# Performance work log

Measured on AMD Instinct MI355X. Metric: run time of the kernel, lower is better.

The kernel has to match this reference:

```python
import jax, jax.numpy as jnp
import numpy as np

NUM_EMB = 8192
DIM = 64
DECAY = 0.99
EPS = 1e-05
COMMIT = 0.25


def setup_inputs() -> dict:
    key = jax.random.key(0)
    k1, k2, k3 = jax.random.split(key, 3)
    inputs = jax.random.normal(k1, (8, 4096, DIM), jnp.float32)
    weight = jax.random.normal(k2, (NUM_EMB, DIM), jnp.float32)
    ema_cluster_count = jnp.ones((NUM_EMB,), jnp.float32)
    ema_weight_sum = jax.random.normal(k3, (NUM_EMB, DIM), jnp.float32)
    return {
        'inputs': inputs,
        'weight': weight,
        'ema_cluster_count': ema_cluster_count,
        'ema_weight_sum': ema_weight_sum,
    }


def reference(inputs, weight, ema_cluster_count, ema_weight_sum):
    flat = inputs.reshape(-1, DIM)  # [N, D]
    distances = (
        jnp.sum(flat ** 2, axis=1, keepdims=True)
        + jnp.sum(weight ** 2, axis=1)
        - 2.0 * flat @ weight.T
    )
    idx = jnp.argmin(distances, axis=1)  # [N] int

    # EMA stats (training branch): one-hot column sums == segment counts,
    # encodings.T @ flat == segment sums of inputs by code index.
    counts = jax.ops.segment_sum(
        jnp.ones(flat.shape[0], jnp.float32), idx, num_segments=NUM_EMB)
    new_cc = ema_cluster_count * DECAY + (1.0 - DECAY) * counts
    emb_sum = jax.ops.segment_sum(flat, idx, num_segments=NUM_EMB)
    new_ws = ema_weight_sum * DECAY + (1.0 - DECAY) * emb_sum

    n = jnp.sum(new_cc)
    smoothed = (new_cc + EPS) / (n + NUM_EMB * EPS) * n
    new_weight = new_ws / smoothed[:, None]  # updated codebook [K, D]

    quantized_raw = new_weight[idx].reshape(inputs.shape)
    e_latent_loss = jnp.mean((jax.lax.stop_gradient(quantized_raw) - inputs) ** 2)
    vq_loss = COMMIT * e_latent_loss

    avg_probs = counts / flat.shape[0]
    perplexity = jnp.exp(-jnp.sum(avg_probs * jnp.log(avg_probs + 1e-10)))

    # straight-through estimator
    quantized = inputs + jax.lax.stop_gradient(quantized_raw - inputs)
    return quantized, vq_loss, idx, perplexity, new_weight, new_cc, new_ws
```

## Files before the change

kernel.cpp:

```cpp
#include <hip/hip_runtime.h>
#include <math.h>

typedef _Float16 f16x8 __attribute__((ext_vector_type(8)));
typedef float f32x4 __attribute__((ext_vector_type(4)));

#define NROWS 32768
#define KEMB  8192

#define DECAYF 0.99f
#define OMDF   0.01f

#define OUT_Q    0
#define OUT_LOSS 2097152
#define OUT_IDX  2097153
#define OUT_PERP 2129921
#define OUT_NW   2129922
#define OUT_NCC  2654210
#define OUT_NWS  2662402

#define WS_N      0
#define WS_ENT    1
#define WS_COUNTS 4
#define WS_EMB    8196
#define WS_IDX    532484
#define WS_W2H    565252
#define WS_WFRAG  573444
#define WS_ZERO_UNITS 532484

__device__ __forceinline__ float sq_rn(float v) { return __fmul_rn(v, v); }

__device__ __forceinline__ float npsumsq64(const float* vbuf) {
  float a[8];
#pragma unroll
  for (int j = 0; j < 8; ++j) a[j] = sq_rn(vbuf[j]);
#pragma unroll
  for (int m = 1; m < 8; ++m)
#pragma unroll
    for (int j = 0; j < 8; ++j) a[j] = __fadd_rn(a[j], sq_rn(vbuf[m*8 + j]));
  return __fadd_rn(__fadd_rn(__fadd_rn(a[0],a[1]), __fadd_rn(a[2],a[3])),
                   __fadd_rn(__fadd_rn(a[4],a[5]), __fadd_rn(a[6],a[7])));
}

__device__ __forceinline__ void split_f16(float x, _Float16& hi, _Float16& lo) {
  hi = (_Float16)x;
  float r = __fsub_rn(x, (float)hi);
  lo = (_Float16)r;
}

__global__ __launch_bounds__(256) void prep_kernel(const float* __restrict__ wg,
                                                   float* __restrict__ ws) {
  const int tid = blockIdx.x * 256 + threadIdx.x;
  if (tid < KEMB) {
    const float* src = wg + (size_t)tid * 64;
    float vbuf[64];
#pragma unroll
    for (int f = 0; f < 16; ++f) {
      float4 v = *(const float4*)(src + f*4);
      vbuf[f*4+0]=v.x; vbuf[f*4+1]=v.y; vbuf[f*4+2]=v.z; vbuf[f*4+3]=v.w;
    }
    ws[WS_W2H + tid] = __fmul_rn(0.5f, npsumsq64(vbuf));
  } else if (tid < KEMB + 65536) {
    const int u = tid - KEMB;
    const int K = u >> 3, g = u & 7;
    const int n = K & 15, P = K >> 4;
    const int slot = (g&3)*16 + n, shi = g >> 2;
    const float* src = wg + (size_t)K*64 + g*8;
    float4 v0 = *(const float4*)src, v1 = *(const float4*)(src + 4);
    float vv[8] = {v0.x,v0.y,v0.z,v0.w,v1.x,v1.y,v1.z,v1.w};
    f16x8 hi, lo;
#pragma unroll
    for (int j = 0; j < 8; ++j) { _Float16 h, l; split_f16(vv[j], h, l); hi[j]=h; lo[j]=l; }
    _Float16* wf = (_Float16*)(ws + WS_WFRAG);
    *(f16x8*)&wf[((size_t)(P*4 + shi)*64 + slot)*8]     = hi;
    *(f16x8*)&wf[((size_t)(P*4 + 2 + shi)*64 + slot)*8] = lo;
  }
}

__global__ __launch_bounds__(1024, 4) void argmin_kernel(const float* __restrict__ xg,
                                                         float* __restrict__ out,
                                                         float* __restrict__ ws) {
  __shared__ __align__(16) _Float16 xp[8*4*64*8];
  __shared__ float md[128*8];
  __shared__ int   mk[128*8];
  __shared__ int   bkL[128];

  const int t    = threadIdx.x;
  const int lane = t & 63, wv = t >> 6;
  const int quad = lane >> 4, n16 = lane & 15;
  const int rg = wv >> 3, cg = wv & 7;
  const int row0 = blockIdx.x * 128;
  const _Float16* __restrict__ wfrag = (const _Float16*)(ws + WS_WFRAG);
  const float* __restrict__ w2hg = ws + WS_W2H;

  {
    const int u  = t;
    const int rp = u >> 7, n = (u >> 3) & 15, g = u & 7;
    const float* src = xg + (size_t)(row0 + rp*16 + n)*64 + g*8;
    float4 v0 = *(const float4*)src, v1 = *(const float4*)(src + 4);
    float vv[8] = {v0.x,v0.y,v0.z,v0.w,v1.x,v1.y,v1.z,v1.w};
    f16x8 hi, lo;
#pragma unroll
    for (int j = 0; j < 8; ++j) { _Float16 h, l; split_f16(-vv[j], h, l); hi[j]=h; lo[j]=l; }
    const int slot = (g&3)*16 + n, shi = g >> 2;
    *(f16x8*)&xp[(((rp*4) + shi)*64 + slot)*8]     = hi;
    *(f16x8*)&xp[(((rp*4) + 2 + shi)*64 + slot)*8] = lo;
  }
  __syncthreads();

  f16x8 b[4][4];
#pragma unroll
  for (int bt = 0; bt < 4; ++bt)
#pragma unroll
    for (int s = 0; s < 4; ++s)
      b[bt][s] = *(const f16x8*)&xp[(((rg*4+bt)*4 + s)*64 + lane)*8];

  float bestd[4]; int bestk[4];
#pragma unroll
  for (int i = 0; i < 4; ++i) { bestd[i] = INFINITY; bestk[i] = 0; }

  const size_t lane8 = (size_t)lane * 8;
  const int q4 = quad * 4;

  f16x8 wh0, wh1, wl0, wl1;
  int kb = cg;
  {
    const size_t base = (size_t)kb * 2048 + lane8;
    wh0 = *(const f16x8*)&wfrag[base];
    wh1 = *(const f16x8*)&wfrag[base + 512];
    wl0 = *(const f16x8*)&wfrag[base + 1024];
    wl1 = *(const f16x8*)&wfrag[base + 1536];
  }
  float4 cw = *(const float4*)&w2hg[kb*16 + q4];

#pragma unroll 1
  for (int it = 0; it < 64; ++it) {
    const f32x4 cin = {cw.x, cw.y, cw.z, cw.w};
    const int c0 = kb*16 + q4;
    f32x4 acc[4];
    __builtin_amdgcn_s_setprio(1);
#pragma unroll
    for (int bt = 0; bt < 4; ++bt) acc[bt] = __builtin_amdgcn_mfma_f32_16x16x32_f16(wh0, b[bt][0], cin,     0,0,0);
#pragma unroll
    for (int bt = 0; bt < 4; ++bt) acc[bt] = __builtin_amdgcn_mfma_f32_16x16x32_f16(wh1, b[bt][1], acc[bt], 0,0,0);
#pragma unroll
    for (int bt = 0; bt < 4; ++bt) acc[bt] = __builtin_amdgcn_mfma_f32_16x16x32_f16(wh0, b[bt][2], acc[bt], 0,0,0);
#pragma unroll
    for (int bt = 0; bt < 4; ++bt) acc[bt] = __builtin_amdgcn_mfma_f32_16x16x32_f16(wh1, b[bt][3], acc[bt], 0,0,0);
#pragma unroll
    for (int bt = 0; bt < 4; ++bt) acc[bt] = __builtin_amdgcn_mfma_f32_16x16x32_f16(wl0, b[bt][0], acc[bt], 0,0,0);
#pragma unroll
    for (int bt = 0; bt < 4; ++bt) acc[bt] = __builtin_amdgcn_mfma_f32_16x16x32_f16(wl1, b[bt][1], acc[bt], 0,0,0);
    __builtin_amdgcn_s_setprio(0);

    if (it < 63) {
      const int pn = kb + 8;
      const size_t base = (size_t)pn * 2048 + lane8;
      wh0 = *(const f16x8*)&wfrag[base];
      wh1 = *(const f16x8*)&wfrag[base + 512];
      wl0 = *(const f16x8*)&wfrag[base + 1024];
      wl1 = *(const f16x8*)&wfrag[base + 1536];
      cw  = *(const float4*)&w2hg[pn*16 + q4];
      kb = pn;
    }

#pragma unroll
    for (int bt = 0; bt < 4; ++bt) {
      const float d0 = acc[bt][0], d1 = acc[bt][1], d2 = acc[bt][2], d3 = acc[bt][3];
      const float pm = fminf(fminf(d0, d1), fminf(d2, d3));
      int koff = 3;
      if (d2 == pm) koff = 2;
      if (d1 == pm) koff = 1;
      if (d0 == pm) koff = 0;
      if (pm < bestd[bt]) { bestd[bt] = pm; bestk[bt] = c0 + koff; }
    }
  }

#pragma unroll
  for (int bt = 0; bt < 4; ++bt) {
    float bd = bestd[bt]; int bk = bestk[bt];
#pragma unroll
    for (int m = 16; m < 64; m <<= 1) {
      const float od = __shfl_xor(bd, m, 64);
      const int   ok = __shfl_xor(bk, m, 64);
      if (od < bd || (od == bd && ok < bk)) { bd = od; bk = ok; }
    }
    if (lane < 16) {
      const int row = rg*64 + bt*16 + n16;
      md[row*8 + cg] = bd;
      mk[row*8 + cg] = bk;
    }
  }
  __syncthreads();

  if (t < 128) {
    const int row = t;
    float bd = md[row*8]; int bk = mk[row*8];
#pragma unroll
    for (int u2 = 1; u2 < 8; ++u2) {
      const float d2 = md[row*8 + u2]; const int k2 = mk[row*8 + u2];
      if (d2 < bd || (d2 == bd && k2 < bk)) { bd = d2; bk = k2; }
    }
    out[OUT_IDX + row0 + row] = (float)bk;
    ((int*)ws)[WS_IDX + row0 + row] = bk;
    bkL[row] = bk;
    atomicAdd(&ws[WS_COUNTS + bk], 1.0f);
  }
  __syncthreads();

#pragma unroll
  for (int r = 0; r < 8; ++r) {
    const int row = wv*8 + r;
    const int k = bkL[row];
    atomicAdd(&ws[WS_EMB + (size_t)k*64 + lane],
              xg[(size_t)(row0 + row)*64 + lane]);
  }
}

__global__ __launch_bounds__(256) void stats_kernel(const float* __restrict__ cc,
                                                    float* __restrict__ out,
                                                    float* __restrict__ ws) {
  const int t = threadIdx.x;
  float v1 = 0.0f, v2 = 0.0f;
#pragma unroll
  for (int i = 0; i < 32; ++i) {
    const int k = i*256 + t;
    const float cnt = ws[WS_COUNTS + k];
    const float ncc = __fadd_rn(__fmul_rn(DECAYF, cc[k]), __fmul_rn(OMDF, cnt));
    out[OUT_NCC + k] = ncc;
    const float p = cnt * (1.0f/32768.0f);
    v1 += ncc;
    v2 += __fmul_rn(p, logf(__fadd_rn(p, 1e-10f)));
  }
#pragma unroll
  for (int off = 32; off > 0; off >>= 1) {
    v1 += __shfl_down(v1, off);
    v2 += __shfl_down(v2, off);
  }
  __shared__ float s1[4], s2[4];
  const int lane = t & 63, wid = t >> 6;
  if (lane == 0) { s1[wid] = v1; s2[wid] = v2; }
  __syncthreads();
  if (t == 0) {
    ws[WS_N]   = (s1[0]+s1[1]) + (s1[2]+s1[3]);
    ws[WS_ENT] = (s2[0]+s2[1]) + (s2[2]+s2[3]);
  }
}

__global__ __launch_bounds__(256) void update_quant_kernel(const float* __restrict__ xg,
                                                           const float* __restrict__ ws0,
                                                           float* __restrict__ out,
                                                           float* __restrict__ ws) {
  const int t = threadIdx.x;
  const float n = ws[WS_N];
  const float den = __fadd_rn(n, 0.08192f);

  const int e4 = blockIdx.x * 256 + t;
  {
    const int k = e4 >> 4;
    const float ncc = out[OUT_NCC + k];
    const float smoothed = __fmul_rn(__fadd_rn(ncc, 1e-5f) / den, n);
    float4 w0 = *(const float4*)(ws0 + (size_t)e4*4);
    float4 em = *(const float4*)(ws + WS_EMB + (size_t)e4*4);
    float wv4[4] = {w0.x, w0.y, w0.z, w0.w};
    float ev4[4] = {em.x, em.y, em.z, em.w};
    float nwsv[4], nwv[4];
#pragma unroll
    for (int i = 0; i < 4; ++i) {
      nwsv[i] = __fadd_rn(__fmul_rn(DECAYF, wv4[i]), __fmul_rn(OMDF, ev4[i]));
      nwv[i]  = nwsv[i] / smoothed;
    }
    float4 onws = {nwsv[0], nwsv[1], nwsv[2], nwsv[3]};
    float4 onw  = {nwv[0],  nwv[1],  nwv[2],  nwv[3]};
    *(float4*)(out + OUT_NWS + (size_t)e4*4) = onws;
    *(float4*)(out + OUT_NW  + (size_t)e4*4) = onw;
    if (e4 == 0) out[OUT_PERP] = expf(-ws[WS_ENT]);
  }

  const int* idxb = (const int*)ws + WS_IDX;
  float v = 0.0f;
#pragma unroll
  for (int j = 0; j < 4; ++j) {
    const int qe4 = (j*512 + blockIdx.x)*256 + t;
    const int row = qe4 >> 4, d = (qe4 & 15) * 4;
    const int k = idxb[row];
    const float ncc = out[OUT_NCC + k];
    const float smK = __fmul_rn(__fadd_rn(ncc, 1e-5f) / den, n);
    float4 wq = *(const float4*)(ws0 + (size_t)k*64 + d);
    float4 eq = *(const float4*)(ws + WS_EMB + (size_t)k*64 + d);
    float4 x  = *(const float4*)(xg + (size_t)qe4*4);
    float wv4[4] = {wq.x,wq.y,wq.z,wq.w};
    float ev4[4] = {eq.x,eq.y,eq.z,eq.w};
    float xv[4]  = {x.x,x.y,x.z,x.w};
    float4 o; float ov[4];
#pragma unroll
    for (int i = 0; i < 4; ++i) {
      const float nws = __fadd_rn(__fmul_rn(DECAYF, wv4[i]), __fmul_rn(OMDF, ev4[i]));
      const float q = nws / smK;
      const float df = __fsub_rn(q, xv[i]);
      ov[i] = __fadd_rn(xv[i], df);
      v = fmaf(df, df, v);
    }
    o.x = ov[0]; o.y = ov[1]; o.z = ov[2]; o.w = ov[3];
    *(float4*)(out + OUT_Q + (size_t)qe4*4) = o;
  }
#pragma unroll
  for (int off = 32; off > 0; off >>= 1) v += __shfl_down(v, off);
  __shared__ float sm[4];
  const int lane = t & 63, wid = t >> 6;
  if (lane == 0) sm[wid] = v;
  __syncthreads();
  if (t == 0) ws[WS_COUNTS + blockIdx.x] = (sm[0]+sm[1]) + (sm[2]+sm[3]);
}

__global__ void final_kernel(float* __restrict__ out, const float* __restrict__ ws) {
  const int t = threadIdx.x;
  float v = 0.0f;
#pragma unroll
  for (int i = 0; i < 8; ++i) v += ws[WS_COUNTS + i*64 + t];
#pragma unroll
  for (int off = 32; off > 0; off >>= 1) v += __shfl_down(v, off);
  if (t == 0) out[OUT_LOSS] = __fmul_rn(0.25f, v / 2097152.0f);
}

extern "C" void kernel_launch(void* const* d_in, const int* in_sizes, int n_in,
                              void* d_out, int out_size, void* d_ws, size_t ws_size,
                              hipStream_t stream) {
  (void)in_sizes; (void)n_in; (void)out_size; (void)ws_size;
  const float* x   = (const float*)d_in[0];
  const float* w   = (const float*)d_in[1];
  const float* cc  = (const float*)d_in[2];
  const float* ws0 = (const float*)d_in[3];
  float* out = (float*)d_out;
  float* ws  = (float*)d_ws;

  hipMemsetAsync(d_ws, 0, (size_t)WS_ZERO_UNITS * 4, stream);
  hipLaunchKernelGGL(prep_kernel,         dim3(288), dim3(256),  0, stream, w, ws);
  hipLaunchKernelGGL(argmin_kernel,       dim3(256), dim3(1024), 0, stream, x, out, ws);
  hipLaunchKernelGGL(stats_kernel,        dim3(1),   dim3(256),  0, stream, cc, out, ws);
  hipLaunchKernelGGL(update_quant_kernel, dim3(512), dim3(256),  0, stream, x, ws0, out, ws);
  hipLaunchKernelGGL(final_kernel,        dim3(1),   dim3(64),   0, stream, out, ws);
}
```

Measured before the change: 179.5 us.

## Fuse memset/stats/final into neighbors and double-buffer MFMA argmin loop

```diff
diff --git a/kernel.cpp b/kernel.cpp
--- a/kernel.cpp
+++ b/kernel.cpp
@@ -20,6 +20,8 @@
 
 #define WS_N      0
 #define WS_ENT    1
+#define WS_CTR    2
+#define WS_CTR2   3
 #define WS_COUNTS 4
 #define WS_EMB    8196
 #define WS_IDX    532484
@@ -50,6 +52,9 @@
 __global__ __launch_bounds__(256) void prep_kernel(const float* __restrict__ wg,
                                                    float* __restrict__ ws) {
   const int tid = blockIdx.x * 256 + threadIdx.x;
+#pragma unroll
+  for (int z = tid; z < WS_ZERO_UNITS; z += 73728) ws[z] = 0.0f;
+
   if (tid < KEMB) {
     const float* src = wg + (size_t)tid * 64;
     float vbuf[64];
@@ -76,13 +81,52 @@
   }
 }
 
-__global__ __launch_bounds__(1024, 4) void argmin_kernel(const float* __restrict__ xg,
-                                                         float* __restrict__ out,
-                                                         float* __restrict__ ws) {
+#define MFMA_CLUSTER(ACC)                                                                     \
+  __builtin_amdgcn_s_setprio(1);                                                              \
+  _Pragma("unroll")                                                                           \
+  for (int bt = 0; bt < 4; ++bt) ACC[bt] = __builtin_amdgcn_mfma_f32_16x16x32_f16(wh0, b[bt][0], cw,      0,0,0); \
+  _Pragma("unroll")                                                                           \
+  for (int bt = 0; bt < 4; ++bt) ACC[bt] = __builtin_amdgcn_mfma_f32_16x16x32_f16(wh1, b[bt][1], ACC[bt], 0,0,0); \
+  _Pragma("unroll")                                                                           \
+  for (int bt = 0; bt < 4; ++bt) ACC[bt] = __builtin_amdgcn_mfma_f32_16x16x32_f16(wh0, b[bt][2], ACC[bt], 0,0,0); \
+  _Pragma("unroll")                                                                           \
+  for (int bt = 0; bt < 4; ++bt) ACC[bt] = __builtin_amdgcn_mfma_f32_16x16x32_f16(wh1, b[bt][3], ACC[bt], 0,0,0); \
+  _Pragma("unroll")                                                                           \
+  for (int bt = 0; bt < 4; ++bt) ACC[bt] = __builtin_amdgcn_mfma_f32_16x16x32_f16(wl0, b[bt][0], ACC[bt], 0,0,0); \
+  _Pragma("unroll")                                                                           \
+  for (int bt = 0; bt < 4; ++bt) ACC[bt] = __builtin_amdgcn_mfma_f32_16x16x32_f16(wl1, b[bt][1], ACC[bt], 0,0,0); \
+  __builtin_amdgcn_s_setprio(0);
+
+#define LOADNEXT()                                  \
+  wh0 = *(const f16x8*)(wp);                        \
+  wh1 = *(const f16x8*)(wp + 512);                  \
+  wl0 = *(const f16x8*)(wp + 1024);                 \
+  wl1 = *(const f16x8*)(wp + 1536);                 \
+  cw  = *(const f32x4*)(cp);                        \
+  wp += 16384; cp += 128;
+
+#define TOURN(ACC, C0)                                                       \
+  _Pragma("unroll")                                                          \
+  for (int bt = 0; bt < 4; ++bt) {                                           \
+    const float d0 = ACC[bt][0], d1 = ACC[bt][1], d2 = ACC[bt][2], d3 = ACC[bt][3]; \
+    const float pm = fminf(fminf(d0, d1), fminf(d2, d3));                    \
+    int koff = 3;                                                            \
+    if (d2 == pm) koff = 2;                                                  \
+    if (d1 == pm) koff = 1;                                                  \
+    if (d0 == pm) koff = 0;                                                  \
+    if (pm < bestd[bt]) { bestd[bt] = pm; bestk[bt] = (C0) + koff; }         \
+  }
+
+__global__ __attribute__((amdgpu_flat_work_group_size(1024,1024), amdgpu_waves_per_eu(4,4)))
+void argmin_kernel(const float* __restrict__ xg, const float* __restrict__ cc,
+                   float* __restrict__ out, float* __restrict__ ws) {
   __shared__ __align__(16) _Float16 xp[8*4*64*8];
   __shared__ float md[128*8];
   __shared__ int   mk[128*8];
   __shared__ int   bkL[128];
+  __shared__ float s1[16], s2[16];
+  __shared__ int   amLast;
+  __shared__ float ldspad[10240];
 
   const int t    = threadIdx.x;
   const int lane = t & 63, wv = t >> 6;
@@ -92,6 +136,11 @@
   const _Float16* __restrict__ wfrag = (const _Float16*)(ws + WS_WFRAG);
   const float* __restrict__ w2hg = ws + WS_W2H;
 
+  if (__float_as_uint(ws[WS_N]) == 0xdeadbeefu) {
+    ldspad[t & 1023] = xg[t];
+    out[OUT_PERP] = ldspad[(t + 1) & 1023];
+  }
+
   {
     const int u  = t;
     const int rp = u >> 7, n = (u >> 3) & 15, g = u & 7;
@@ -118,62 +167,37 @@
 #pragma unroll
   for (int i = 0; i < 4; ++i) { bestd[i] = INFINITY; bestk[i] = 0; }
 
-  const size_t lane8 = (size_t)lane * 8;
-  const int q4 = quad * 4;
-
-  f16x8 wh0, wh1, wl0, wl1;
-  int kb = cg;
-  {
-    const size_t base = (size_t)kb * 2048 + lane8;
-    wh0 = *(const f16x8*)&wfrag[base];
-    wh1 = *(const f16x8*)&wfrag[base + 512];
-    wl0 = *(const f16x8*)&wfrag[base + 1024];
-    wl1 = *(const f16x8*)&wfrag[base + 1536];
-  }
-  float4 cw = *(const float4*)&w2hg[kb*16 + q4];
+  const _Float16* wp = wfrag + (size_t)cg * 2048 + (size_t)lane * 8;
+  const float*    cp = w2hg + cg*16 + quad*4;
+
+  f16x8 wh0 = *(const f16x8*)(wp);
+  f16x8 wh1 = *(const f16x8*)(wp + 512);
+  f16x8 wl0 = *(const f16x8*)(wp + 1024);
+  f16x8 wl1 = *(const f16x8*)(wp + 1536);
+  f32x4 cw  = *(const f32x4*)(cp);
+  wp += 16384; cp += 128;
+
+  f32x4 accA[4], accB[4];
+  int c0A = cg*16 + quad*4, c0B;
+
+  MFMA_CLUSTER(accA);
+  LOADNEXT();
 
 #pragma unroll 1
-  for (int it = 0; it < 64; ++it) {
-    const f32x4 cin = {cw.x, cw.y, cw.z, cw.w};
-    const int c0 = kb*16 + q4;
-    f32x4 acc[4];
-    __builtin_amdgcn_s_setprio(1);
-#pragma unroll
-    for (int bt = 0; bt < 4; ++bt) acc[bt] = __builtin_amdgcn_mfma_f32_16x16x32_f16(wh0, b[bt][0], cin,     0,0,0);
-#pragma unroll
-    for (int bt = 0; bt < 4; ++bt) acc[bt] = __builtin_amdgcn_mfma_f32_16x16x32_f16(wh1, b[bt][1], acc[bt], 0,0,0);
-#pragma unroll
-    for (int bt = 0; bt < 4; ++bt) acc[bt] = __builtin_amdgcn_mfma_f32_16x16x32_f16(wh0, b[bt][2], acc[bt], 0,0,0);
-#pragma unroll
-    for (int bt = 0; bt < 4; ++bt) acc[bt] = __builtin_amdgcn_mfma_f32_16x16x32_f16(wh1, b[bt][3], acc[bt], 0,0,0);
-#pragma unroll
-    for (int bt = 0; bt < 4; ++bt) acc[bt] = __builtin_amdgcn_mfma_f32_16x16x32_f16(wl0, b[bt][0], acc[bt], 0,0,0);
-#pragma unroll
-    for (int bt = 0; bt < 4; ++bt) acc[bt] = __builtin_amdgcn_mfma_f32_16x16x32_f16(wl1, b[bt][1], acc[bt], 0,0,0);
-    __builtin_amdgcn_s_setprio(0);
-
-    if (it < 63) {
-      const int pn = kb + 8;
-      const size_t base = (size_t)pn * 2048 + lane8;
-      wh0 = *(const f16x8*)&wfrag[base];
-      wh1 = *(const f16x8*)&wfrag[base + 512];
-      wl0 = *(const f16x8*)&wfrag[base + 1024];
-      wl1 = *(const f16x8*)&wfrag[base + 1536];
-      cw  = *(const float4*)&w2hg[pn*16 + q4];
-      kb = pn;
-    }
-
-#pragma unroll
-    for (int bt = 0; bt < 4; ++bt) {
-      const float d0 = acc[bt][0], d1 = acc[bt][1], d2 = acc[bt][2], d3 = acc[bt][3];
-      const float pm = fminf(fminf(d0, d1), fminf(d2, d3));
-      int koff = 3;
-      if (d2 == pm) koff = 2;
-      if (d1 == pm) koff = 1;
-      if (d0 == pm) koff = 0;
-      if (pm < bestd[bt]) { bestd[bt] = pm; bestk[bt] = c0 + koff; }
-    }
-  }
+  for (int j = 0; j < 31; ++j) {
+    MFMA_CLUSTER(accB);
+    c0B = c0A + 128;
+    LOADNEXT();
+    TOURN(accA, c0A);
+    MFMA_CLUSTER(accA);
+    c0A = c0B + 128;
+    LOADNEXT();
+    TOURN(accB, c0B);
+  }
+  MFMA_CLUSTER(accB);
+  c0B = c0A + 128;
+  TOURN(accA, c0A);
+  TOURN(accB, c0B);
 
 #pragma unroll
   for (int bt = 0; bt < 4; ++bt) {
@@ -214,35 +238,37 @@
     atomicAdd(&ws[WS_EMB + (size_t)k*64 + lane],
               xg[(size_t)(row0 + row)*64 + lane]);
   }
-}
-
-__global__ __launch_bounds__(256) void stats_kernel(const float* __restrict__ cc,
-                                                    float* __restrict__ out,
-                                                    float* __restrict__ ws) {
-  const int t = threadIdx.x;
-  float v1 = 0.0f, v2 = 0.0f;
-#pragma unroll
-  for (int i = 0; i < 32; ++i) {
-    const int k = i*256 + t;
-    const float cnt = ws[WS_COUNTS + k];
-    const float ncc = __fadd_rn(__fmul_rn(DECAYF, cc[k]), __fmul_rn(OMDF, cnt));
-    out[OUT_NCC + k] = ncc;
-    const float p = cnt * (1.0f/32768.0f);
-    v1 += ncc;
-    v2 += __fmul_rn(p, logf(__fadd_rn(p, 1e-10f)));
-  }
-#pragma unroll
-  for (int off = 32; off > 0; off >>= 1) {
-    v1 += __shfl_down(v1, off);
-    v2 += __shfl_down(v2, off);
-  }
-  __shared__ float s1[4], s2[4];
-  const int lane = t & 63, wid = t >> 6;
-  if (lane == 0) { s1[wid] = v1; s2[wid] = v2; }
-  __syncthreads();
-  if (t == 0) {
-    ws[WS_N]   = (s1[0]+s1[1]) + (s1[2]+s1[3]);
-    ws[WS_ENT] = (s2[0]+s2[1]) + (s2[2]+s2[3]);
+
+  __threadfence();
+  if (t == 0) amLast = (atomicAdd((int*)ws + WS_CTR, 1) == (int)gridDim.x - 1);
+  __syncthreads();
+  if (amLast) {
+    __threadfence();
+    float v1 = 0.0f, v2 = 0.0f;
+#pragma unroll
+    for (int i = 0; i < 8; ++i) {
+      const int k = i*1024 + t;
+      const float cnt = ws[WS_COUNTS + k];
+      const float ncc = __fadd_rn(__fmul_rn(DECAYF, cc[k]), __fmul_rn(OMDF, cnt));
+      out[OUT_NCC + k] = ncc;
+      const float p = cnt * (1.0f/32768.0f);
+      v1 += ncc;
+      v2 += __fmul_rn(p, logf(__fadd_rn(p, 1e-10f)));
+    }
+#pragma unroll
+    for (int off = 32; off > 0; off >>= 1) {
+      v1 += __shfl_down(v1, off);
+      v2 += __shfl_down(v2, off);
+    }
+    if (lane == 0) { s1[wv] = v1; s2[wv] = v2; }
+    __syncthreads();
+    if (t == 0) {
+      float a1 = 0.0f, a2 = 0.0f;
+#pragma unroll
+      for (int i = 0; i < 16; ++i) { a1 += s1[i]; a2 += s2[i]; }
+      ws[WS_N]   = a1;
+      ws[WS_ENT] = a2;
+    }
   }
 }
 
@@ -250,6 +276,8 @@
                                                            const float* __restrict__ ws0,
                                                            float* __restrict__ out,
                                                            float* __restrict__ ws) {
+  __shared__ float sm[4];
+  __shared__ int amL;
   const int t = threadIdx.x;
   const float n = ws[WS_N];
   const float den = __fadd_rn(n, 0.08192f);
@@ -305,21 +333,25 @@
   }
 #pragma unroll
   for (int off = 32; off > 0; off >>= 1) v += __shfl_down(v, off);
-  __shared__ float sm[4];
   const int lane = t & 63, wid = t >> 6;
   if (lane == 0) sm[wid] = v;
   __syncthreads();
   if (t == 0) ws[WS_COUNTS + blockIdx.x] = (sm[0]+sm[1]) + (sm[2]+sm[3]);
-}
-
-__global__ void final_kernel(float* __restrict__ out, const float* __restrict__ ws) {
-  const int t = threadIdx.x;
-  float v = 0.0f;
-#pragma unroll
-  for (int i = 0; i < 8; ++i) v += ws[WS_COUNTS + i*64 + t];
-#pragma unroll
-  for (int off = 32; off > 0; off >>= 1) v += __shfl_down(v, off);
-  if (t == 0) out[OUT_LOSS] = __fmul_rn(0.25f, v / 2097152.0f);
+
+  __threadfence();
+  if (t == 0) amL = (atomicAdd((int*)ws + WS_CTR2, 1) == (int)gridDim.x - 1);
+  __syncthreads();
+  if (amL) {
+    __threadfence();
+    if (t < 64) {
+      float vv = 0.0f;
+#pragma unroll
+      for (int i = 0; i < 8; ++i) vv += ws[WS_COUNTS + i*64 + t];
+#pragma unroll
+      for (int off = 32; off > 0; off >>= 1) vv += __shfl_down(vv, off);
+      if (t == 0) out[OUT_LOSS] = __fmul_rn(0.25f, vv / 2097152.0f);
+    }
+  }
 }
 
 extern "C" void kernel_launch(void* const* d_in, const int* in_sizes, int n_in,
@@ -333,10 +365,7 @@
   float* out = (float*)d_out;
   float* ws  = (float*)d_ws;
 
-  hipMemsetAsync(d_ws, 0, (size_t)WS_ZERO_UNITS * 4, stream);
   hipLaunchKernelGGL(prep_kernel,         dim3(288), dim3(256),  0, stream, w, ws);
-  hipLaunchKernelGGL(argmin_kernel,       dim3(256), dim3(1024), 0, stream, x, out, ws);
-  hipLaunchKernelGGL(stats_kernel,        dim3(1),   dim3(256),  0, stream, cc, out, ws);
+  hipLaunchKernelGGL(argmin_kernel,       dim3(256), dim3(1024), 0, stream, x, cc, out, ws);
   hipLaunchKernelGGL(update_quant_kernel, dim3(512), dim3(256),  0, stream, x, ws0, out, ws);
-  hipLaunchKernelGGL(final_kernel,        dim3(1),   dim3(64),   0, stream, out, ws);
-}
+}
```

After: 300.2 us. +67.3%, slower.
